# Optimization experiments

Hardware: AMD Instinct MI355X
Metric: run time of the kernel (lower is better)

## Reference

```python
import jax, jax.numpy as jnp
import numpy as np

H = 8        # num_heads
DK = 128     # head_k_dim
DV = 128     # head_v_dim
HID = 1024   # hidden_size
CHUNK = 64   # chunk size for chunked linear attention
EPS = 1e-5


def setup_inputs() -> dict:
    key = jax.random.key(0)
    ks = jax.random.split(key, 16)
    s = 0.02
    inp = {
        "hidden_states": jax.random.normal(ks[0], (2, 8192, HID), dtype=jnp.float32),
        "Wq": jax.random.normal(ks[1], (HID, HID), dtype=jnp.float32) * s,
        "Wk": jax.random.normal(ks[2], (HID, HID), dtype=jnp.float32) * s,
        "Wv": jax.random.normal(ks[3], (HID, HID), dtype=jnp.float32) * s,
        "fmq_w1": jax.random.normal(ks[4], (DK, DK), dtype=jnp.float32) * s,
        "fmq_b1": jnp.zeros((DK,), dtype=jnp.float32),
        "fmq_w2": jax.random.normal(ks[5], (DK, DK), dtype=jnp.float32) * s,
        "fmq_b2": jnp.zeros((DK,), dtype=jnp.float32),
        "fmk_w1": jax.random.normal(ks[6], (DK, DK), dtype=jnp.float32) * s,
        "fmk_b1": jnp.zeros((DK,), dtype=jnp.float32),
        "fmk_w2": jax.random.normal(ks[7], (DK, DK), dtype=jnp.float32) * s,
        "fmk_b2": jnp.zeros((DK,), dtype=jnp.float32),
        "rms_w": jnp.ones((DV,), dtype=jnp.float32),
        "Wo": jax.random.normal(ks[8], (HID, HID), dtype=jnp.float32) * s,
    }
    return inp


def reference(hidden_states, Wq, Wk, Wv, fmq_w1, fmq_b1, fmq_w2, fmq_b2,
              fmk_w1, fmk_b1, fmk_w2, fmk_b2, rms_w, Wo):
    B, T, _ = hidden_states.shape
    scale = DK ** -0.5

    # projections (torch Linear: x @ W.T), split heads -> [B,T,H,D]
    q = (hidden_states @ Wq.T).reshape(B, T, H, DK)
    k = (hidden_states @ Wk.T).reshape(B, T, H, DK)
    v = (hidden_states @ Wv.T).reshape(B, T, H, DV)

    # Hadamard feature maps: l1(x) * l2(x)
    q = (q @ fmq_w1.T + fmq_b1) * (q @ fmq_w2.T + fmq_b2)
    k = (k @ fmk_w1.T + fmk_b1) * (k @ fmk_w2.T + fmk_b2)

    q = q * scale

    # chunked causal linear attention: o_t = q_t @ sum_{s<=t} k_s v_s^T
    N = T // CHUNK
    qc = q.reshape(B, N, CHUNK, H, DK)
    kc = k.reshape(B, N, CHUNK, H, DK)
    vc = v.reshape(B, N, CHUNK, H, DV)

    # per-chunk KV outer-product sums, exclusive prefix over chunks
    kv = jnp.einsum('bnchk,bnchv->bnhkv', kc, vc)
    S = jnp.cumsum(kv, axis=1) - kv  # state entering each chunk

    o_inter = jnp.einsum('bnchk,bnhkv->bnchv', qc, S)

    # intra-chunk causal part
    A = jnp.einsum('bnihk,bnjhk->bnhij', qc, kc)
    causal = jnp.tril(jnp.ones((CHUNK, CHUNK), dtype=bool))
    A = jnp.where(causal, A, 0.0)
    o_intra = jnp.einsum('bnhij,bnjhv->bnihv', A, vc)

    o = (o_inter + o_intra).reshape(B, T, H, DV)

    # RMSNorm over head_v_dim with affine weight
    o = o * jax.lax.rsqrt(jnp.mean(o * o, axis=-1, keepdims=True) + EPS) * rms_w

    o = o.reshape(B, T, H * DV) @ Wo.T
    return o
```

## Files before the change

### kernel.cpp

```cpp
#include <hip/hip_runtime.h>


typedef __bf16 bf16x8 __attribute__((ext_vector_type(8)));
typedef float  f32x4  __attribute__((ext_vector_type(4)));

__device__ __forceinline__ float bf2f(unsigned short u) {
  union { unsigned int i; float f; } v; v.i = ((unsigned int)u) << 16; return v.f;
}
__device__ __forceinline__ unsigned short f2bf(float f) {
  union { float f; unsigned int i; } v; v.f = f;
  return (unsigned short)((v.i + 0x8000u) >> 16);
}
__device__ __forceinline__ unsigned int pk2(float a, float b) {
  union { float f; unsigned int i; } x, y; x.f = a; y.f = b;
  return ((x.i + 0x8000u) >> 16) | ((y.i + 0x8000u) & 0xFFFF0000u);
}
__device__ __forceinline__ f32x4 mfma16(bf16x8 a, bf16x8 b, f32x4 c) {
  return __builtin_amdgcn_mfma_f32_16x16x32_bf16(a, b, c, 0, 0, 0);
}
__device__ __forceinline__ void gl_lds16(const unsigned short* g, unsigned short* l) {
  __builtin_amdgcn_global_load_lds((const __attribute__((address_space(1))) void*)g,
                                   (__attribute__((address_space(3))) void*)l, 16, 0, 0);
}

__global__ void __launch_bounds__(256)
cvt_all(const float* __restrict__ X,
        const float* __restrict__ W0, const float* __restrict__ W1,
        const float* __restrict__ W2, const float* __restrict__ W3,
        const float* __restrict__ F0, const float* __restrict__ F1,
        const float* __restrict__ F2, const float* __restrict__ F3,
        unsigned short* __restrict__ Xd,
        unsigned short* __restrict__ W0d, unsigned short* __restrict__ W1d,
        unsigned short* __restrict__ W2d, unsigned short* __restrict__ W3d,
        unsigned short* __restrict__ F0d, unsigned short* __restrict__ F1d,
        unsigned short* __restrict__ F2d, unsigned short* __restrict__ F3d) {
  const int i = blockIdx.x * 256 + threadIdx.x;
  const float* s; unsigned short* d; int off;
  if (i < 4194304) { s = X; d = Xd; off = i; }
  else {
    int i2 = i - 4194304;
    if (i2 < 1048576) {
      const int w = i2 >> 18; off = i2 & 262143;
      s = (w == 0) ? W0 : (w == 1) ? W1 : (w == 2) ? W2 : W3;
      d = (w == 0) ? W0d : (w == 1) ? W1d : (w == 2) ? W2d : W3d;
    } else {
      int i3 = i2 - 1048576;
      if (i3 >= 16384) return;
      const int w = i3 >> 12; off = i3 & 4095;
      s = (w == 0) ? F0 : (w == 1) ? F1 : (w == 2) ? F2 : F3;
      d = (w == 0) ? F0d : (w == 1) ? F1d : (w == 2) ? F2d : F3d;
    }
  }
  const float4 f = ((const float4*)s)[off];
  uint2 o; o.x = pk2(f.x, f.y); o.y = pk2(f.z, f.w);
  ((uint2*)d)[off] = o;
}

__device__ __forceinline__ int stage_goff(int s) {
  const int j = s >> 3, c = (s & 7) ^ (j & 7);
  return (2 * j + (c >> 2)) * 1024 + (c & 3) * 8;
}

__device__ __forceinline__ void gemm256_loop(const unsigned short* __restrict__ gA,
                                             const unsigned short* __restrict__ gB,
                                             unsigned short* __restrict__ ldsA,
                                             unsigned short* __restrict__ ldsB,
                                             int tid, f32x4 (&acc)[8][4]) {
  const int lane = tid & 63, wid = tid >> 6;
  const int lq = lane & 15, quad = lane >> 4;
  const int wm = (wid >> 2) * 128, wn = (wid & 3) * 64;

  const unsigned short* gA0 = gA + stage_goff(tid);
  const unsigned short* gA1 = gA + stage_goff(512 + tid);
  const unsigned short* gB0 = gB + stage_goff(tid);
  const unsigned short* gB1 = gB + stage_goff(512 + tid);
  const int l0 = wid * 512;
  const int l1 = 4096 + wid * 512;
  const int soff = (lq >> 1) * 64 + (((((lq & 1) << 2) + quad) ^ ((lq >> 1) & 7))) * 8;

#pragma unroll
  for (int h = 0; h < 3; ++h) {
    gl_lds16(gA0 + h * 32, ldsA + h * 8192 + l0);
    gl_lds16(gA1 + h * 32, ldsA + h * 8192 + l1);
    gl_lds16(gB0 + h * 32, ldsB + h * 8192 + l0);
    gl_lds16(gB1 + h * 32, ldsB + h * 8192 + l1);
  }
  asm volatile("s_waitcnt vmcnt(4)" ::: "memory");
  __builtin_amdgcn_s_barrier();
  __builtin_amdgcn_sched_barrier(0);

  bf16x8 pa[2][8], pb[2][4];
#pragma unroll
  for (int f = 0; f < 8; ++f)
    pa[0][f] = *(const bf16x8*)(ldsA + (wm + f * 16) * 32 + soff);
#pragma unroll
  for (int g = 0; g < 4; ++g)
    pb[0][g] = *(const bf16x8*)(ldsB + (wn + g * 16) * 32 + soff);

#pragma unroll
  for (int u = 0; u < 32; ++u) {
    const int cur = u & 1, nxt = cur ^ 1;
    if (u > 0) {
      if (u < 30) asm volatile("s_waitcnt vmcnt(4)" ::: "memory");
      else        asm volatile("s_waitcnt vmcnt(0)" ::: "memory");
      __builtin_amdgcn_s_barrier();
      __builtin_amdgcn_sched_barrier(0);
    }
    if (u < 29) {
      unsigned short* sa = ldsA + ((u + 3) & 3) * 8192;
      unsigned short* sb = ldsB + ((u + 3) & 3) * 8192;
      gl_lds16(gA0 + (u + 3) * 32, sa + l0);
      gl_lds16(gA1 + (u + 3) * 32, sa + l1);
      gl_lds16(gB0 + (u + 3) * 32, sb + l0);
      gl_lds16(gB1 + (u + 3) * 32, sb + l1);
    }
    if (u < 31) {
      const unsigned short* An = ldsA + ((u + 1) & 3) * 8192;
      const unsigned short* Bn = ldsB + ((u + 1) & 3) * 8192;
#pragma unroll
      for (int f = 0; f < 8; ++f)
        pa[nxt][f] = *(const bf16x8*)(An + (wm + f * 16) * 32 + soff);
#pragma unroll
      for (int g = 0; g < 4; ++g)
        pb[nxt][g] = *(const bf16x8*)(Bn + (wn + g * 16) * 32 + soff);
    }
    __builtin_amdgcn_s_setprio(1);
#pragma unroll
    for (int f = 0; f < 8; ++f)
#pragma unroll
      for (int g = 0; g < 4; ++g)
        acc[f][g] = mfma16(pa[cur][f], pb[cur][g], acc[f][g]);
    __builtin_amdgcn_s_setprio(0);
  }
}

__global__ void __launch_bounds__(512, 2)
qkv_gemm256(const unsigned short* __restrict__ Xb, const unsigned short* __restrict__ Bw,
            unsigned short* __restrict__ Cq, unsigned short* __restrict__ VT, int sel) {
  extern __shared__ unsigned short lds[];
  const int tid = threadIdx.x;
  const int bx = blockIdx.x;
  const int tm = (bx & 7) * 8 + ((bx >> 3) & 7);
  const int ct = bx >> 6;
  const int rowBase = tm * 256, colBase = ct * 256;

  f32x4 acc[8][4] = {};
  gemm256_loop(Xb + (size_t)rowBase * 1024, Bw + (size_t)colBase * 1024,
               lds, lds + 32768, tid, acc);

  const int lane = tid & 63, wid = tid >> 6;
  const int lq = lane & 15, quad = lane >> 4;
  const int wm = (wid >> 2) * 128, wn = (wid & 3) * 64;
  if (sel < 2) {
#pragma unroll
    for (int f = 0; f < 8; ++f)
#pragma unroll
      for (int g = 0; g < 4; ++g) {
        const int col = colBase + wn + g * 16 + lq;
#pragma unroll
        for (int r = 0; r < 4; ++r) {
          const int row = rowBase + wm + f * 16 + quad * 4 + r;
          Cq[(size_t)row * 1024 + col] = f2bf(acc[f][g][r]);
        }
      }
  } else {
#pragma unroll
    for (int f = 0; f < 8; ++f)
#pragma unroll
      for (int g = 0; g < 4; ++g) {
        const int col = colBase + wn + g * 16 + lq;
        const int h = col >> 7, dv = col & 127;
        const int row0 = rowBase + wm + f * 16 + quad * 4;
        const int b = row0 >> 13, tl = row0 & 8191;
        ushort4 t4;
        t4.x = f2bf(acc[f][g][0]); t4.y = f2bf(acc[f][g][1]);
        t4.z = f2bf(acc[f][g][2]); t4.w = f2bf(acc[f][g][3]);
        *(ushort4*)(VT + (((size_t)(b * 8 + h) * 128 + dv) << 13) + tl) = t4;
      }
  }
}

__global__ void __launch_bounds__(512, 2)
out_gemm256(const unsigned short* __restrict__ A, const unsigned short* __restrict__ Bw,
            float* __restrict__ C) {
  extern __shared__ unsigned short lds[];
  const int tid = threadIdx.x;
  const int bx = blockIdx.x;
  const int tm = (bx & 7) * 8 + ((bx >> 3) & 7);
  const int tn = bx >> 6;
  const int rowBase = tm * 256, colBase = tn * 256;

  f32x4 acc[8][4] = {};
  gemm256_loop(A + (size_t)rowBase * 1024, Bw + (size_t)colBase * 1024,
               lds, lds + 32768, tid, acc);

  const int lane = tid & 63, wid = tid >> 6;
  const int lq = lane & 15, quad = lane >> 4;
  const int wm = (wid >> 2) * 128, wn = (wid & 3) * 64;
#pragma unroll
  for (int f = 0; f < 8; ++f)
#pragma unroll
    for (int g = 0; g < 4; ++g) {
      const int col = colBase + wn + g * 16 + lq;
#pragma unroll
      for (int r = 0; r < 4; ++r) {
        const int row = rowBase + wm + f * 16 + quad * 4 + r;
        C[(size_t)row * 1024 + col] = acc[f][g][r];
      }
    }
}

__global__ void __launch_bounds__(256)
fm_kernel(unsigned short* __restrict__ Qb, unsigned short* __restrict__ Kb,
          const unsigned short* __restrict__ fq1b, const unsigned short* __restrict__ fq2b,
          const unsigned short* __restrict__ fk1b, const unsigned short* __restrict__ fk2b,
          const float* __restrict__ fqb1, const float* __restrict__ fqb2,
          const float* __restrict__ fkb1, const float* __restrict__ fkb2) {
  __shared__ unsigned short Aq[64 * 136];
  const int z = blockIdx.z;
  unsigned short* buf = z ? Kb : Qb;
  const unsigned short* w1b = z ? fk1b : fq1b;
  const unsigned short* w2b = z ? fk2b : fq2b;
  const float* b1 = z ? fkb1 : fqb1;
  const float* b2 = z ? fkb2 : fqb2;
  const float scale = z ? 1.0f : 0.08838834764831843f;

  const int tid = threadIdx.x;
  const int t0 = blockIdx.x * 256;
  const int h = blockIdx.y, hc = h * 128;
  const int lane = tid & 63, wid = tid >> 6, lq = lane & 15, quad = lane >> 4;
  const int wn = wid * 32;

  bf16x8 w1f[4][2], w2f[4][2];
#pragma unroll
  for (int ks = 0; ks < 4; ++ks)
#pragma unroll
    for (int j = 0; j < 2; ++j) {
      const int nr = wn + j * 16 + lq;
      w1f[ks][j] = *(const bf16x8*)(w1b + nr * 128 + ks * 32 + quad * 8);
      w2f[ks][j] = *(const bf16x8*)(w2b + nr * 128 + ks * 32 + quad * 8);
    }

  const float bb1[2] = { b1[wn + lq], b1[wn + 16 + lq] };
  const float bb2[2] = { b2[wn + lq], b2[wn + 16 + lq] };

  for (int tt = 0; tt < 4; ++tt) {
    const int tb = t0 + tt * 64;
#pragma unroll
    for (int it = 0; it < 4; ++it) {
      const int p = tid + it * 256;
      const int row = p >> 4, c8 = (p & 15) * 8;
      *(uint4*)(Aq + row * 136 + c8) =
          *(const uint4*)(buf + (size_t)(tb + row) * 1024 + hc + c8);
    }
    __syncthreads();
    f32x4 a1[4][2] = {}, a2[4][2] = {};
#pragma unroll
    for (int ks = 0; ks < 4; ++ks) {
      bf16x8 af[4];
#pragma unroll
      for (int i = 0; i < 4; ++i)
        af[i] = *(const bf16x8*)(Aq + (i * 16 + lq) * 136 + ks * 32 + quad * 8);
#pragma unroll
      for (int j = 0; j < 2; ++j)
#pragma unroll
        for (int i = 0; i < 4; ++i) {
          a1[i][j] = mfma16(af[i], w1f[ks][j], a1[i][j]);
          a2[i][j] = mfma16(af[i], w2f[ks][j], a2[i][j]);
        }
    }
    __syncthreads();
#pragma unroll
    for (int j = 0; j < 2; ++j) {
      const int col = wn + j * 16 + lq;
#pragma unroll
      for (int i = 0; i < 4; ++i)
#pragma unroll
        for (int r = 0; r < 4; ++r) {
          const float v = (a1[i][j][r] + bb1[j]) * (a2[i][j][r] + bb2[j]) * scale;
          buf[(size_t)(tb + i * 16 + quad * 4 + r) * 1024 + hc + col] = f2bf(v);
        }
    }
  }
}

__global__ void __launch_bounds__(256)
kv_kernel(const unsigned short* __restrict__ Kf, const unsigned short* __restrict__ VT,
          unsigned short* __restrict__ KV) {
  __shared__ unsigned short Kt[128 * 72];
  __shared__ unsigned short Vt[128 * 72];
  const int tid = threadIdx.x;
  const int n = blockIdx.x, bh = blockIdx.y;
  const int b = bh >> 3, h = bh & 7;
  const int t0g = b * 8192 + n * 64;
  const int tl0 = n * 64;
#pragma unroll
  for (int it = 0; it < 4; ++it) {
    const int p = tid + it * 256;
    const int d = p >> 3, c8 = (p & 7) * 8;
    *(uint4*)(Vt + d * 72 + c8) =
        *(const uint4*)(VT + (((size_t)bh * 128 + d) << 13) + tl0 + c8);
    const int tok = p >> 4, c8k = (p & 15) * 8;
    const unsigned short* src = Kf + (size_t)(t0g + tok) * 1024 + h * 128 + c8k;
    ushort4 k0 = *(const ushort4*)(src);
    ushort4 k1 = *(const ushort4*)(src + 4);
    Kt[(c8k + 0) * 72 + tok] = k0.x; Kt[(c8k + 1) * 72 + tok] = k0.y;
    Kt[(c8k + 2) * 72 + tok] = k0.z; Kt[(c8k + 3) * 72 + tok] = k0.w;
    Kt[(c8k + 4) * 72 + tok] = k1.x; Kt[(c8k + 5) * 72 + tok] = k1.y;
    Kt[(c8k + 6) * 72 + tok] = k1.z; Kt[(c8k + 7) * 72 + tok] = k1.w;
  }
  __syncthreads();
  const int lane = tid & 63, wid = tid >> 6, lq = lane & 15, quad = lane >> 4;
  const int wm = (wid >> 1) * 64, wn = (wid & 1) * 64;
  f32x4 acc[4][4] = {};
#pragma unroll
  for (int ks = 0; ks < 2; ++ks) {
    bf16x8 af[4], bfr[4];
#pragma unroll
    for (int i = 0; i < 4; ++i)
      af[i] = *(const bf16x8*)(Vt + (wm + i * 16 + lq) * 72 + ks * 32 + quad * 8);
#pragma unroll
    for (int j = 0; j < 4; ++j)
      bfr[j] = *(const bf16x8*)(Kt + (wn + j * 16 + lq) * 72 + ks * 32 + quad * 8);
#pragma unroll
    for (int i = 0; i < 4; ++i)
#pragma unroll
      for (int j = 0; j < 4; ++j) acc[i][j] = mfma16(af[i], bfr[j], acc[i][j]);
  }
  const size_t base = ((size_t)bh * 128 + n) * 16384;
#pragma unroll
  for (int i = 0; i < 4; ++i)
#pragma unroll
    for (int j = 0; j < 4; ++j)
#pragma unroll
      for (int r = 0; r < 4; ++r)
        KV[base + (size_t)(wm + i * 16 + quad * 4 + r) * 128 + wn + j * 16 + lq] =
            f2bf(acc[i][j][r]);
}

__global__ void __launch_bounds__(256)
cumsum_kernel(unsigned short* __restrict__ KV) {
  const int idx = blockIdx.x * 256 + threadIdx.x;
  const int bh = idx >> 14, e = idx & 16383;
  unsigned short* p = KV + (size_t)bh * (128 * 16384) + e;
  float run = 0.f;
  for (int nb = 0; nb < 16; ++nb) {
    unsigned short x[8];
#pragma unroll
    for (int i = 0; i < 8; ++i) x[i] = p[(size_t)i * 16384];
#pragma unroll
    for (int i = 0; i < 8; ++i) {
      const float v = bf2f(x[i]);
      p[(size_t)i * 16384] = f2bf(run);
      run += v;
    }
    p += (size_t)8 * 16384;
  }
}

__global__ void __launch_bounds__(256)
attn_kernel(const unsigned short* __restrict__ Q, const unsigned short* __restrict__ Kf,
            const unsigned short* __restrict__ VT, const unsigned short* __restrict__ S,
            const float* __restrict__ rmsw, unsigned short* __restrict__ O) {
  __shared__ uint4 smem4[3968];
  unsigned short* sm = (unsigned short*)smem4;
  unsigned short* SQ = sm;
  unsigned short* KS = sm + 8704;
  unsigned short* VTl = sm + 17920;
  unsigned short* AL = sm + 27136;
  float* OL = (float*)sm;
  float* RED = (float*)AL;
  float* SCL = RED + 256;

  const int tid = threadIdx.x;
  const int n = blockIdx.x, bh = blockIdx.y;
  const int b = bh >> 3, h = bh & 7;
  const int t0g = b * 8192 + n * 64;
  const int tl0 = n * 64;
  const int lane = tid & 63, wid = tid >> 6, lq = lane & 15, quad = lane >> 4;

  const size_t sbase = ((size_t)bh * 128 + n) * 16384;
  bf16x8 sfr[2][2][2];
#pragma unroll
  for (int hh = 0; hh < 2; ++hh)
#pragma unroll
    for (int ks = 0; ks < 2; ++ks)
#pragma unroll
      for (int j = 0; j < 2; ++j)
        sfr[hh][ks][j] = *(const bf16x8*)(S + sbase +
            (size_t)(wid * 32 + j * 16 + lq) * 128 + hh * 64 + ks * 32 + quad * 8);

#pragma unroll
  for (int it = 0; it < 4; ++it) {
    const int p = tid + it * 256;
    const int row = p >> 4, c8 = (p & 15) * 8;
    *(uint4*)(SQ + row * 136 + c8) =
        *(const uint4*)(Q + (size_t)(t0g + row) * 1024 + h * 128 + c8);
    *(uint4*)(KS + row * 136 + c8) =
        *(const uint4*)(Kf + (size_t)(t0g + row) * 1024 + h * 128 + c8);
    const int d = p >> 3, c8b = (p & 7) * 8;
    *(uint4*)(VTl + d * 72 + c8b) =
        *(const uint4*)(VT + (((size_t)bh * 128 + d) << 13) + tl0 + c8b);
  }
  __syncthreads();

  {
    f32x4 aa[4] = {};
#pragma unroll
    for (int ks = 0; ks < 4; ++ks) {
      bf16x8 kf = *(const bf16x8*)(KS + (wid * 16 + lq) * 136 + ks * 32 + quad * 8);
#pragma unroll
      for (int i = 0; i < 4; ++i) {
        bf16x8 qf = *(const bf16x8*)(SQ + (i * 16 + lq) * 136 + ks * 32 + quad * 8);
        aa[i] = mfma16(qf, kf, aa[i]);
      }
    }
#pragma unroll
    for (int i = 0; i < 4; ++i)
#pragma unroll
      for (int r = 0; r < 4; ++r) {
        const int qp = i * 16 + quad * 4 + r, kp = wid * 16 + lq;
        AL[qp * 72 + kp] = f2bf(kp <= qp ? aa[i][r] : 0.f);
      }
  }
  __syncthreads();

  f32x4 oa[4][2] = {};
#pragma unroll
  for (int ks = 0; ks < 2; ++ks) {
    bf16x8 bv[2];
#pragma unroll
    for (int j = 0; j < 2; ++j)
      bv[j] = *(const bf16x8*)(VTl + (wid * 32 + j * 16 + lq) * 72 + ks * 32 + quad * 8);
#pragma unroll
    for (int i = 0; i < 4; ++i) {
      bf16x8 af  = *(const bf16x8*)(AL + (i * 16 + lq) * 72 + ks * 32 + quad * 8);
      bf16x8 qf0 = *(const bf16x8*)(SQ + (i * 16 + lq) * 136 + ks * 32 + quad * 8);
      bf16x8 qf1 = *(const bf16x8*)(SQ + (i * 16 + lq) * 136 + (ks + 2) * 32 + quad * 8);
#pragma unroll
      for (int j = 0; j < 2; ++j) {
        oa[i][j] = mfma16(af, bv[j], oa[i][j]);
        oa[i][j] = mfma16(qf0, sfr[0][ks][j], oa[i][j]);
        oa[i][j] = mfma16(qf1, sfr[1][ks][j], oa[i][j]);
      }
    }
  }
  __syncthreads();

#pragma unroll
  for (int i = 0; i < 4; ++i)
#pragma unroll
    for (int j = 0; j < 2; ++j)
#pragma unroll
      for (int r = 0; r < 4; ++r)
        OL[(i * 16 + quad * 4 + r) * 132 + wid * 32 + j * 16 + lq] = oa[i][j][r];
  __syncthreads();

  {
    const int r = tid >> 2, part = tid & 3;
    const float* pr = OL + r * 132 + part * 32;
    float s = 0.f;
#pragma unroll
    for (int c = 0; c < 32; ++c) { const float v = pr[c]; s += v * v; }
    RED[r * 4 + part] = s;
  }
  __syncthreads();
  if (tid < 64) {
    const float ms = (RED[tid * 4] + RED[tid * 4 + 1] + RED[tid * 4 + 2] + RED[tid * 4 + 3]) *
                     (1.f / 128.f);
    SCL[tid] = rsqrtf(ms + 1e-5f);
  }
  __syncthreads();

#pragma unroll
  for (int it = 0; it < 4; ++it) {
    const int r = (tid >> 4) + it * 16;
    const int c8 = (tid & 15) * 8;
    const float sc = SCL[r];
    unsigned short us[8];
#pragma unroll
    for (int e = 0; e < 8; ++e)
      us[e] = f2bf(OL[r * 132 + c8 + e] * sc * rmsw[c8 + e]);
    uint4 pk;
    pk.x = (unsigned int)us[0] | ((unsigned int)us[1] << 16);
    pk.y = (unsigned int)us[2] | ((unsigned int)us[3] << 16);
    pk.z = (unsigned int)us[4] | ((unsigned int)us[5] << 16);
    pk.w = (unsigned int)us[6] | ((unsigned int)us[7] << 16);
    *(uint4*)(O + (size_t)(t0g + r) * 1024 + h * 128 + c8) = pk;
  }
}

extern "C" void kernel_launch(void* const* d_in, const int* in_sizes, int n_in,
                              void* d_out, int out_size, void* d_ws, size_t ws_size,
                              hipStream_t stream) {
  const float* X    = (const float*)d_in[0];
  const float* Wq   = (const float*)d_in[1];
  const float* Wk   = (const float*)d_in[2];
  const float* Wv   = (const float*)d_in[3];
  const float* fq1  = (const float*)d_in[4];
  const float* fqb1 = (const float*)d_in[5];
  const float* fq2  = (const float*)d_in[6];
  const float* fqb2 = (const float*)d_in[7];
  const float* fk1  = (const float*)d_in[8];
  const float* fkb1 = (const float*)d_in[9];
  const float* fk2  = (const float*)d_in[10];
  const float* fkb2 = (const float*)d_in[11];
  const float* rmsw = (const float*)d_in[12];
  const float* Wo   = (const float*)d_in[13];

  static bool attr_done = false;
  if (!attr_done) {
    (void)hipFuncSetAttribute((const void*)qkv_gemm256,
                              hipFuncAttributeMaxDynamicSharedMemorySize, 131072);
    (void)hipFuncSetAttribute((const void*)out_gemm256,
                              hipFuncAttributeMaxDynamicSharedMemorySize, 131072);
    attr_done = true;
  }

  const size_t MB = 1u << 20;
  char* ws = (char*)d_ws;
  unsigned short* Q    = (unsigned short*)(ws);
  unsigned short* Kf   = (unsigned short*)(ws + 32 * MB);
  unsigned short* VT   = (unsigned short*)(ws + 64 * MB);
  unsigned short* KV   = (unsigned short*)(ws + 96 * MB);
  unsigned short* Xb   = KV;
  unsigned short* Wqb  = (unsigned short*)(ws + 160 * MB);
  unsigned short* Wkb  = (unsigned short*)(ws + 162 * MB);
  unsigned short* Wvb  = (unsigned short*)(ws + 164 * MB);
  unsigned short* Wob  = (unsigned short*)(ws + 166 * MB);
  unsigned short* fq1b = (unsigned short*)(ws + 168 * MB);
  unsigned short* fq2b = fq1b + 16384;
  unsigned short* fk1b = fq1b + 32768;
  unsigned short* fk2b = fq1b + 49152;
  unsigned short* O    = Q;

  cvt_all<<<20544, 256, 0, stream>>>(X, Wq, Wk, Wv, Wo, fq1, fq2, fk1, fk2,
                                     Xb, Wqb, Wkb, Wvb, Wob,
                                     fq1b, fq2b, fk1b, fk2b);

  qkv_gemm256<<<dim3(256), dim3(512), 131072, stream>>>(Xb, Wqb, Q, VT, 0);
  qkv_gemm256<<<dim3(256), dim3(512), 131072, stream>>>(Xb, Wkb, Kf, VT, 1);
  qkv_gemm256<<<dim3(256), dim3(512), 131072, stream>>>(Xb, Wvb, Q, VT, 2);
  fm_kernel<<<dim3(64, 8, 2), 256, 0, stream>>>(Q, Kf, fq1b, fq2b, fk1b, fk2b,
                                                fqb1, fqb2, fkb1, fkb2);
  kv_kernel<<<dim3(128, 16), 256, 0, stream>>>(Kf, VT, KV);
  cumsum_kernel<<<1024, 256, 0, stream>>>(KV);
  attn_kernel<<<dim3(128, 16), 256, 0, stream>>>(Q, Kf, VT, KV, rmsw, O);
  out_gemm256<<<dim3(256), dim3(512), 131072, stream>>>(O, Wob, (float*)d_out);
}
```

Before: 394.7 us.

## Vectorize cumsum, shrink attention LDS footprint, remap output GEMM tile order

```diff
diff --git a/kernel.cpp b/kernel.cpp
--- a/kernel.cpp
+++ b/kernel.cpp
@@ -186,8 +186,8 @@
   extern __shared__ unsigned short lds[];
   const int tid = threadIdx.x;
   const int bx = blockIdx.x;
-  const int tm = (bx & 7) * 8 + ((bx >> 3) & 7);
-  const int tn = bx >> 6;
+  const int l = (bx & 7) * 32 + (bx >> 3);
+  const int tm = l & 63, tn = l >> 6;
   const int rowBase = tm * 256, colBase = tn * 256;
 
   f32x4 acc[8][4] = {};
@@ -341,18 +341,21 @@
 __global__ void __launch_bounds__(256)
 cumsum_kernel(unsigned short* __restrict__ KV) {
   const int idx = blockIdx.x * 256 + threadIdx.x;
-  const int bh = idx >> 14, e = idx & 16383;
-  unsigned short* p = KV + (size_t)bh * (128 * 16384) + e;
-  float run = 0.f;
+  const int bh = idx >> 12, e4 = (idx & 4095) * 4;
+  unsigned short* p = KV + (size_t)bh * (128 * 16384) + e4;
+  float run0 = 0.f, run1 = 0.f, run2 = 0.f, run3 = 0.f;
   for (int nb = 0; nb < 16; ++nb) {
-    unsigned short x[8];
-#pragma unroll
-    for (int i = 0; i < 8; ++i) x[i] = p[(size_t)i * 16384];
+    ushort4 x[8];
+#pragma unroll
+    for (int i = 0; i < 8; ++i) x[i] = *(const ushort4*)(p + (size_t)i * 16384);
 #pragma unroll
     for (int i = 0; i < 8; ++i) {
-      const float v = bf2f(x[i]);
-      p[(size_t)i * 16384] = f2bf(run);
-      run += v;
+      ushort4 o;
+      o.x = f2bf(run0); run0 += bf2f(x[i].x);
+      o.y = f2bf(run1); run1 += bf2f(x[i].y);
+      o.z = f2bf(run2); run2 += bf2f(x[i].z);
+      o.w = f2bf(run3); run3 += bf2f(x[i].w);
+      *(ushort4*)(p + (size_t)i * 16384) = o;
     }
     p += (size_t)8 * 16384;
   }
@@ -362,14 +365,13 @@
 attn_kernel(const unsigned short* __restrict__ Q, const unsigned short* __restrict__ Kf,
             const unsigned short* __restrict__ VT, const unsigned short* __restrict__ S,
             const float* __restrict__ rmsw, unsigned short* __restrict__ O) {
-  __shared__ uint4 smem4[3968];
-  unsigned short* sm = (unsigned short*)smem4;
-  unsigned short* SQ = sm;
-  unsigned short* KS = sm + 8704;
-  unsigned short* VTl = sm + 17920;
-  unsigned short* AL = sm + 27136;
-  float* OL = (float*)sm;
-  float* RED = (float*)AL;
+  __shared__ unsigned short smx[26624];
+  unsigned short* SQ = smx;
+  unsigned short* KS = smx + 8704;
+  unsigned short* AL = KS;
+  unsigned short* VTl = smx + 17408;
+  float* OL = (float*)smx;
+  float* RED = (float*)(smx + 17408);
   float* SCL = RED + 256;
 
   const int tid = threadIdx.x;
@@ -415,6 +417,7 @@
         aa[i] = mfma16(qf, kf, aa[i]);
       }
     }
+    __syncthreads();
 #pragma unroll
     for (int i = 0; i < 4; ++i)
 #pragma unroll
@@ -544,7 +547,7 @@
   fm_kernel<<<dim3(64, 8, 2), 256, 0, stream>>>(Q, Kf, fq1b, fq2b, fk1b, fk2b,
                                                 fqb1, fqb2, fkb1, fkb2);
   kv_kernel<<<dim3(128, 16), 256, 0, stream>>>(Kf, VT, KV);
-  cumsum_kernel<<<1024, 256, 0, stream>>>(KV);
+  cumsum_kernel<<<256, 256, 0, stream>>>(KV);
   attn_kernel<<<dim3(128, 16), 256, 0, stream>>>(Q, Kf, VT, KV, rmsw, O);
   out_gemm256<<<dim3(256), dim3(512), 131072, stream>>>(O, Wob, (float*)d_out);
 }
```

After: 400.4 us. No clear change (+1.4%).
